# Kernel optimization log

Measured on AMD Instinct MI355X. Metric: run time of the kernel, lower is better.

## Reference

```python
import jax, jax.numpy as jnp
import numpy as np

COS_EPS = 1e-6   # torch CosineSimilarity eps
NORM_EPS = 1e-10 # assignment-normalizer eps


def setup_inputs() -> dict:
    key = jax.random.key(0)
    ks = jax.random.split(key, 12)
    s = 0.1
    H, K, Din, Dout = 8, 128, 64, 64
    return {
        "node_set": jax.random.normal(ks[0], (32, Din, 1024, 12), jnp.float32),
        "adj": jax.random.uniform(ks[1], (32, 1024, 1024), jnp.float32),
        "W0": jax.random.normal(ks[2], (Din, Din), jnp.float32) * s,
        "w_i2c": jax.random.normal(ks[3], (H, 1), jnp.float32) * s,
        "b_i2c": jax.random.normal(ks[4], (H,), jnp.float32) * s,
        "W_lin": jax.random.normal(ks[5], (H * K, H), jnp.float32) * s,
        "b_lin": jax.random.normal(ks[6], (H * K,), jnp.float32) * s,
        "conv_w": jax.random.normal(ks[7], (H,), jnp.float32) * s,
        "conv_b": jax.random.normal(ks[8], (), jnp.float32) * s,
        "W_feat": jax.random.normal(ks[9], (Dout, Din), jnp.float32) * s,
        "b_feat": jax.random.normal(ks[10], (Dout,), jnp.float32) * s,
    }


def reference(node_set, adj, W0, w_i2c, b_i2c, W_lin, b_lin, conv_w, conv_b, W_feat, b_feat):
    # [B, C, N, T] -> [B, N, C, T] -> mean over T -> [B, N, D]
    x = jnp.mean(jnp.transpose(node_set, (0, 2, 1, 3)), axis=3)
    B = x.shape[0]
    H = w_i2c.shape[0]
    K = W_lin.shape[0] // H

    # get_att: attention-pooled global centroid seed [B, 1, D]
    temp = jnp.mean(x, axis=1, keepdims=True)                 # [B,1,D]
    h_avg = jnp.tanh(jnp.einsum('bod,de->boe', temp, W0))    # [B,1,D]
    att = jnp.einsum('bnd,bod->bno', x, h_avg)               # [B,N,1]
    cent = jnp.einsum('bno,bnd->bod', att, x)                # [B,1,D]

    # generate batch centroids: [B,D,1] -> [B,D,H] -> [B,D,H*K] -> [B,H,K,D]
    bc = jnp.transpose(cent, (0, 2, 1))                       # [B,D,1]
    bc = jax.nn.relu(bc @ w_i2c.T + b_i2c)                    # [B,D,H]
    bc = jax.nn.relu(bc @ W_lin.T + b_lin)                    # [B,D,H*K]
    bc = jnp.transpose(bc, (0, 2, 1)).reshape(B, H, K, -1)    # [B,H,K,D]

    # cosine-similarity assignment (no 5D repeat: dot / max(|x||c|, eps))
    dots = jnp.einsum('bnd,bhkd->bhkn', x, bc)                # [B,H,K,N]
    xn = jnp.linalg.norm(x, axis=-1)                          # [B,N]
    cn = jnp.linalg.norm(bc, axis=-1)                         # [B,H,K]
    C_heads = dots / jnp.maximum(cn[..., None] * xn[:, None, None, :], COS_EPS)
    # normalize over centroids dim (dim 2)
    C_heads = C_heads / (jnp.sum(C_heads, axis=2, keepdims=True) + NORM_EPS)

    # 1x1 conv over heads -> single assignment matrix [B,K,N]
    C = jnp.einsum('h,bhkn->bkn', conv_w, C_heads) + conv_b

    # pooled node features + output projection
    new_node_set = jnp.einsum('bkn,bnd->bkd', C, x)           # [B,K,D]
    return new_node_set @ W_feat.T + b_feat                   # [B,K,Dout]
```

## Files before the change

### kernel.cpp

```cpp
#include <hip/hip_runtime.h>
#include <math.h>

#define B_  32
#define N_  1024
#define D_  64
#define H_  8
#define K_  128
#define HK_ 1024

__global__ __launch_bounds__(512) void k1_mean(const float* __restrict__ ns,
        float* __restrict__ x, float* __restrict__ invxn,
        float* __restrict__ part1) {
    __shared__ float tile[64][65];
    int b    = blockIdx.x >> 4;
    int n0   = (blockIdx.x & 15) << 6;
    int lane = threadIdx.x & 63;
    int w    = threadIdx.x >> 6;
    #pragma unroll
    for (int j = 0; j < 8; ++j) {
        int d = w * 8 + j;
        const float4* p = (const float4*)(ns +
            ((size_t)((b * 64 + d) * 1024 + n0 + lane)) * 12);
        float4 a = p[0], c = p[1], e = p[2];
        float s = ((a.x + a.y) + (a.z + a.w)) + ((c.x + c.y) + (c.z + c.w))
                + ((e.x + e.y) + (e.z + e.w));
        tile[lane][d] = s * (1.0f / 12.0f);
    }
    __syncthreads();
    #pragma unroll
    for (int j = 0; j < 8; ++j) {
        int r = w * 8 + j;
        float v = tile[r][lane];
        x[((size_t)(b * 1024 + n0 + r)) * 64 + lane] = v;
        float ss = v * v;
        #pragma unroll
        for (int o = 32; o; o >>= 1) ss += __shfl_xor(ss, o);
        if (lane == 0) invxn[b * 1024 + n0 + r] = 1.0f / sqrtf(fmaxf(ss, 1e-30f));
    }
    if (threadIdx.x < 64) {
        float s = 0.0f;
        #pragma unroll 16
        for (int r = 0; r < 64; ++r) s += tile[r][threadIdx.x];
        part1[(size_t)blockIdx.x * 64 + threadIdx.x] = s;
    }
}

__global__ __launch_bounds__(256) void k3_cent(const float* __restrict__ x,
        const float* __restrict__ part1, const float* __restrict__ W0,
        float* __restrict__ part2) {
    __shared__ float t[64];
    __shared__ float ha[64];
    __shared__ float cp[4][64];
    int b    = blockIdx.x >> 2;
    int n0   = (blockIdx.x & 3) << 8;
    int lane = threadIdx.x & 63;
    int w    = threadIdx.x >> 6;
    if (threadIdx.x < 64) {
        float s = 0.0f;
        #pragma unroll
        for (int j = 0; j < 16; ++j) s += part1[(size_t)(b * 16 + j) * 64 + threadIdx.x];
        t[threadIdx.x] = s * (1.0f / 1024.0f);
    }
    __syncthreads();
    if (threadIdx.x < 64) {
        float a = 0.0f;
        #pragma unroll 8
        for (int d = 0; d < 64; ++d) a += t[d] * W0[d * 64 + threadIdx.x];
        ha[threadIdx.x] = tanhf(a);
    }
    __syncthreads();
    float hv = ha[lane];
    float cw = 0.0f;
    for (int nn = w; nn < 256; nn += 4) {
        float xv = x[((size_t)(b * 1024 + n0 + nn)) * 64 + lane];
        float d  = xv * hv;
        #pragma unroll
        for (int o = 32; o; o >>= 1) d += __shfl_xor(d, o);
        cw += d * xv;
    }
    cp[w][lane] = cw;
    __syncthreads();
    if (w == 0)
        part2[(size_t)blockIdx.x * 64 + lane] =
            ((cp[0][lane] + cp[1][lane]) + (cp[2][lane] + cp[3][lane]));
}

__global__ __launch_bounds__(256) void k4_bc(const float* __restrict__ part2,
        const float* __restrict__ w_i2c, const float* __restrict__ b_i2c,
        const float* __restrict__ W_lin, const float* __restrict__ b_lin,
        float* __restrict__ bc, float* __restrict__ invcn) {
    int lane = threadIdx.x & 63;
    int w    = threadIdx.x >> 6;
    int gg   = blockIdx.x * 4 + w;
    int b    = gg >> 8;
    int kk0  = (gg & 255) * 4;
    float c = 0.0f;
    #pragma unroll
    for (int s = 0; s < 4; ++s) c += part2[(size_t)(b * 4 + s) * 64 + lane];
    float b1[8];
    #pragma unroll
    for (int h = 0; h < 8; ++h) b1[h] = fmaxf(c * w_i2c[h] + b_i2c[h], 0.0f);
    #pragma unroll
    for (int u = 0; u < 4; ++u) {
        int kk = kk0 + u;
        float pre = b_lin[kk];
        #pragma unroll
        for (int h = 0; h < 8; ++h) pre += b1[h] * W_lin[kk * 8 + h];
        float v = fmaxf(pre, 0.0f);
        bc[((size_t)(b * 1024 + kk)) * 64 + lane] = v;
        float ss = v * v;
        #pragma unroll
        for (int o = 32; o; o >>= 1) ss += __shfl_xor(ss, o);
        if (lane == 0) invcn[b * 1024 + kk] = (ss > 0.0f) ? (1.0f / sqrtf(ss)) : 0.0f;
    }
}

__global__ __launch_bounds__(256, 2) void k5_assign(const float* __restrict__ x,
        const float* __restrict__ bc, const float* __restrict__ invxn,
        const float* __restrict__ invcn, const float* __restrict__ conv_w,
        const float* __restrict__ conv_b, float* __restrict__ C) {
    __shared__ float xt[64][68];
    __shared__ float bct[128][68];
    __shared__ float invx_s[64];
    __shared__ float invc_s[128];
    __shared__ float sred[16][68];
    int b   = blockIdx.x >> 4;
    int n0  = (blockIdx.x & 15) << 6;
    int tid = threadIdx.x;
    {
        int r = tid >> 2, dh = (tid & 3) << 4;
        const float4* src = (const float4*)(x + ((size_t)(b * 1024 + n0 + r)) * 64 + dh);
        float4* dst = (float4*)(&xt[r][dh]);
        dst[0] = src[0]; dst[1] = src[1]; dst[2] = src[2]; dst[3] = src[3];
    }
    if (tid < 64) invx_s[tid] = invxn[b * 1024 + n0 + tid];
    {
        int r = tid >> 1, dh = (tid & 1) << 5;
        const float4* src = (const float4*)(bc + ((size_t)(b * 1024 + r)) * 64 + dh);
        float4* dst = (float4*)(&bct[r][dh]);
        #pragma unroll
        for (int u = 0; u < 8; ++u) dst[u] = src[u];
    }
    if (tid < 128) invc_s[tid] = invcn[b * 1024 + tid];
    float Cacc[8][4];
    #pragma unroll
    for (int i = 0; i < 8; ++i)
        #pragma unroll
        for (int j = 0; j < 4; ++j) Cacc[i][j] = 0.0f;
    int q = tid >> 4, p = tid & 15;
    float cb = conv_b[0];
    int rr = tid >> 1, dhh = (tid & 1) << 5;
    for (int h = 0; h < 8; ++h) {
        __syncthreads();
        int hn = (h + 1) & 7;
        float4 pf[8];
        float  pfc = 0.0f;
        {
            const float4* src = (const float4*)(bc + ((size_t)(b * 1024 + hn * 128 + rr)) * 64 + dhh);
            #pragma unroll
            for (int u = 0; u < 8; ++u) pf[u] = src[u];
        }
        if (tid < 128) pfc = invcn[b * 1024 + hn * 128 + tid];
        float acc[8][4];
        #pragma unroll
        for (int i = 0; i < 8; ++i)
            #pragma unroll
            for (int j = 0; j < 4; ++j) acc[i][j] = 0.0f;
        for (int dc = 0; dc < 64; dc += 4) {
            float4 bv[8], xv[4];
            #pragma unroll
            for (int i = 0; i < 8; ++i) bv[i] = *(const float4*)(&bct[q + 16 * i][dc]);
            #pragma unroll
            for (int j = 0; j < 4; ++j) xv[j] = *(const float4*)(&xt[p + 16 * j][dc]);
            #pragma unroll
            for (int i = 0; i < 8; ++i)
                #pragma unroll
                for (int j = 0; j < 4; ++j)
                    acc[i][j] += bv[i].x * xv[j].x + bv[i].y * xv[j].y
                               + bv[i].z * xv[j].z + bv[i].w * xv[j].w;
        }
        float part[4];
        #pragma unroll
        for (int j = 0; j < 4; ++j) part[j] = 0.0f;
        #pragma unroll
        for (int i = 0; i < 8; ++i) {
            float ic = invc_s[q + 16 * i];
            #pragma unroll
            for (int j = 0; j < 4; ++j) {
                float v = acc[i][j] * ic * invx_s[p + 16 * j];
                acc[i][j] = v;
                part[j] += v;
            }
        }
        #pragma unroll
        for (int j = 0; j < 4; ++j) sred[q][p + 16 * j] = part[j];
        __syncthreads();
        {
            float4* dst = (float4*)(&bct[rr][dhh]);
            #pragma unroll
            for (int u = 0; u < 8; ++u) dst[u] = pf[u];
        }
        if (tid < 128) invc_s[tid] = pfc;
        float cwv = conv_w[h];
        #pragma unroll
        for (int j = 0; j < 4; ++j) {
            float s = 0.0f;
            #pragma unroll
            for (int qq = 0; qq < 16; ++qq) s += sred[qq][p + 16 * j];
            float si = 1.0f / (s + 1e-10f);
            #pragma unroll
            for (int i = 0; i < 8; ++i) Cacc[i][j] += cwv * acc[i][j] * si;
        }
    }
    #pragma unroll
    for (int i = 0; i < 8; ++i) {
        int k = q + 16 * i;
        #pragma unroll
        for (int j = 0; j < 4; ++j)
            C[((size_t)(b * 128 + k)) * 1024 + n0 + p + 16 * j] = Cacc[i][j] + cb;
    }
}

__global__ __launch_bounds__(256, 2) void k6_out(const float* __restrict__ C,
        const float* __restrict__ x, const float* __restrict__ Wf,
        const float* __restrict__ bfeat, float* __restrict__ out) {
    __shared__ float xt[128][68];
    __shared__ float ct[16][132];
    __shared__ float nnst[16][68];
    __shared__ float wfs[64][68];
    int b   = blockIdx.x >> 3;
    int k0  = (blockIdx.x & 7) << 4;
    int tid = threadIdx.x;
    int kq  = tid >> 4, p = tid & 15;
    for (int t = tid; t < 4096; t += 256) wfs[t >> 6][t & 63] = Wf[t];
    float acc[4] = {0.0f, 0.0f, 0.0f, 0.0f};
    for (int c = 0; c < 8; ++c) {
        __syncthreads();
        {
            int r = tid >> 1, dh = (tid & 1) << 5;
            const float4* src = (const float4*)(x + ((size_t)(b * 1024 + c * 128 + r)) * 64 + dh);
            float4* dst = (float4*)(&xt[r][dh]);
            #pragma unroll
            for (int u = 0; u < 8; ++u) dst[u] = src[u];
        }
        for (int t = tid; t < 2048; t += 256)
            ct[t >> 7][t & 127] = C[((size_t)(b * 128 + k0 + (t >> 7))) * 1024 + c * 128 + (t & 127)];
        __syncthreads();
        #pragma unroll 8
        for (int n = 0; n < 128; ++n) {
            float  cv = ct[kq][n];
            float4 xv = *(const float4*)(&xt[n][p << 2]);
            acc[0] += cv * xv.x; acc[1] += cv * xv.y;
            acc[2] += cv * xv.z; acc[3] += cv * xv.w;
        }
    }
    __syncthreads();
    nnst[kq][(p << 2) + 0] = acc[0];
    nnst[kq][(p << 2) + 1] = acc[1];
    nnst[kq][(p << 2) + 2] = acc[2];
    nnst[kq][(p << 2) + 3] = acc[3];
    __syncthreads();
    float o0 = bfeat[(p << 2) + 0], o1 = bfeat[(p << 2) + 1];
    float o2 = bfeat[(p << 2) + 2], o3 = bfeat[(p << 2) + 3];
    #pragma unroll
    for (int dc = 0; dc < 64; dc += 4) {
        float4 nv = *(const float4*)(&nnst[kq][dc]);
        float4 w0 = *(const float4*)(&wfs[(p << 2) + 0][dc]);
        float4 w1 = *(const float4*)(&wfs[(p << 2) + 1][dc]);
        float4 w2 = *(const float4*)(&wfs[(p << 2) + 2][dc]);
        float4 w3 = *(const float4*)(&wfs[(p << 2) + 3][dc]);
        o0 += nv.x * w0.x + nv.y * w0.y + nv.z * w0.z + nv.w * w0.w;
        o1 += nv.x * w1.x + nv.y * w1.y + nv.z * w1.z + nv.w * w1.w;
        o2 += nv.x * w2.x + nv.y * w2.y + nv.z * w2.z + nv.w * w2.w;
        o3 += nv.x * w3.x + nv.y * w3.y + nv.z * w3.z + nv.w * w3.w;
    }
    float4 ov = make_float4(o0, o1, o2, o3);
    *(float4*)(out + ((size_t)(b * 128 + k0 + kq)) * 64 + (p << 2)) = ov;
}

extern "C" void kernel_launch(void* const* d_in, const int* in_sizes, int n_in,
                              void* d_out, int out_size, void* d_ws, size_t ws_size,
                              hipStream_t stream) {
    const float* node_set = (const float*)d_in[0];
    const float* W0     = (const float*)d_in[2];
    const float* w_i2c  = (const float*)d_in[3];
    const float* b_i2c  = (const float*)d_in[4];
    const float* W_lin  = (const float*)d_in[5];
    const float* b_lin  = (const float*)d_in[6];
    const float* conv_w = (const float*)d_in[7];
    const float* conv_b = (const float*)d_in[8];
    const float* W_feat = (const float*)d_in[9];
    const float* b_feat = (const float*)d_in[10];
    float* out = (float*)d_out;
    float* ws  = (float*)d_ws;

    float* x     = ws;
    float* invxn = ws + 2097152;
    float* part1 = ws + 2129920;
    float* part2 = ws + 2162688;
    float* bc    = ws + 2170880;
    float* invcn = ws + 4268032;
    float* Cmat  = ws + 4300800;

    k1_mean  <<<B_ * 16, 512, 0, stream>>>(node_set, x, invxn, part1);
    k3_cent  <<<B_ * 4,  256, 0, stream>>>(x, part1, W0, part2);
    k4_bc    <<<2048,    256, 0, stream>>>(part2, w_i2c, b_i2c, W_lin, b_lin, bc, invcn);
    k5_assign<<<B_ * 16, 256, 0, stream>>>(x, bc, invxn, invcn, conv_w, conv_b, Cmat);
    k6_out   <<<B_ * 8,  256, 0, stream>>>(Cmat, x, W_feat, b_feat, out);
}
```

Before: 419.1 us.

## Enlarge assign tile to 128 nodes with async LDS double-buffered centroid loads

```diff
diff --git a/kernel.cpp b/kernel.cpp
--- a/kernel.cpp
+++ b/kernel.cpp
@@ -7,6 +7,9 @@
 #define H_  8
 #define K_  128
 #define HK_ 1024
+
+#define GLB(p) ((const __attribute__((address_space(1))) void*)(p))
+#define LDSP(p) ((__attribute__((address_space(3))) void*)(p))
 
 __global__ __launch_bounds__(512) void k1_mean(const float* __restrict__ ns,
         float* __restrict__ x, float* __restrict__ invxn,
@@ -51,8 +54,8 @@
     __shared__ float t[64];
     __shared__ float ha[64];
     __shared__ float cp[4][64];
-    int b    = blockIdx.x >> 2;
-    int n0   = (blockIdx.x & 3) << 8;
+    int b    = blockIdx.x >> 3;
+    int n0   = (blockIdx.x & 7) << 7;
     int lane = threadIdx.x & 63;
     int w    = threadIdx.x >> 6;
     if (threadIdx.x < 64) {
@@ -71,7 +74,7 @@
     __syncthreads();
     float hv = ha[lane];
     float cw = 0.0f;
-    for (int nn = w; nn < 256; nn += 4) {
+    for (int nn = w; nn < 128; nn += 4) {
         float xv = x[((size_t)(b * 1024 + n0 + nn)) * 64 + lane];
         float d  = xv * hv;
         #pragma unroll
@@ -96,7 +99,7 @@
     int kk0  = (gg & 255) * 4;
     float c = 0.0f;
     #pragma unroll
-    for (int s = 0; s < 4; ++s) c += part2[(size_t)(b * 4 + s) * 64 + lane];
+    for (int s = 0; s < 8; ++s) c += part2[(size_t)(b * 8 + s) * 64 + lane];
     float b1[8];
     #pragma unroll
     for (int h = 0; h < 8; ++h) b1[h] = fmaxf(c * w_i2c[h] + b_i2c[h], 0.0f);
@@ -115,108 +118,141 @@
     }
 }
 
-__global__ __launch_bounds__(256, 2) void k5_assign(const float* __restrict__ x,
+__global__ __launch_bounds__(256, 1) void k5_assign(const float* __restrict__ x,
         const float* __restrict__ bc, const float* __restrict__ invxn,
         const float* __restrict__ invcn, const float* __restrict__ conv_w,
         const float* __restrict__ conv_b, float* __restrict__ C) {
-    __shared__ float xt[64][68];
-    __shared__ float bct[128][68];
-    __shared__ float invx_s[64];
-    __shared__ float invc_s[128];
-    __shared__ float sred[16][68];
-    int b   = blockIdx.x >> 4;
-    int n0  = (blockIdx.x & 15) << 6;
+    __shared__ float xt[128][68];
+    __shared__ float bct[2][128 * 64];
+    __shared__ float invx_s[128];
+    __shared__ float invc_s[2][128];
+    __shared__ float sredW[128][4];
+    int b   = blockIdx.x >> 3;
+    int n0  = (blockIdx.x & 7) << 7;
     int tid = threadIdx.x;
+    int l   = tid & 63, w = tid >> 6;
+    int q   = tid >> 4, p = tid & 15;
+    int rxor = q & 7;
+    int rl  = l >> 4, cl = l & 15;
     {
-        int r = tid >> 2, dh = (tid & 3) << 4;
+        int r = tid >> 1, dh = (tid & 1) << 5;
         const float4* src = (const float4*)(x + ((size_t)(b * 1024 + n0 + r)) * 64 + dh);
         float4* dst = (float4*)(&xt[r][dh]);
-        dst[0] = src[0]; dst[1] = src[1]; dst[2] = src[2]; dst[3] = src[3];
-    }
-    if (tid < 64) invx_s[tid] = invxn[b * 1024 + n0 + tid];
+        #pragma unroll
+        for (int u = 0; u < 8; ++u) dst[u] = src[u];
+    }
+    if (tid < 128) {
+        invx_s[tid]    = invxn[b * 1024 + n0 + tid];
+        invc_s[0][tid] = invcn[b * 1024 + tid];
+    }
     {
-        int r = tid >> 1, dh = (tid & 1) << 5;
-        const float4* src = (const float4*)(bc + ((size_t)(b * 1024 + r)) * 64 + dh);
-        float4* dst = (float4*)(&bct[r][dh]);
-        #pragma unroll
-        for (int u = 0; u < 8; ++u) dst[u] = src[u];
-    }
-    if (tid < 128) invc_s[tid] = invcn[b * 1024 + tid];
-    float Cacc[8][4];
+        const float* hb = bc + ((size_t)(b * 1024)) * 64;
+        #pragma unroll
+        for (int t = 0; t < 8; ++t) {
+            int chunk = w * 8 + t;
+            int r = chunk * 4 + rl;
+            const float* src = hb + (size_t)r * 64 + ((cl ^ (r & 7)) << 2);
+            __builtin_amdgcn_global_load_lds(GLB(src), LDSP(&bct[0][chunk * 256]), 16, 0, 0);
+        }
+    }
+    float Cacc[8][8];
     #pragma unroll
     for (int i = 0; i < 8; ++i)
         #pragma unroll
-        for (int j = 0; j < 4; ++j) Cacc[i][j] = 0.0f;
-    int q = tid >> 4, p = tid & 15;
+        for (int j = 0; j < 8; ++j) Cacc[i][j] = 0.0f;
     float cb = conv_b[0];
-    int rr = tid >> 1, dhh = (tid & 1) << 5;
+    __syncthreads();
+
     for (int h = 0; h < 8; ++h) {
-        __syncthreads();
-        int hn = (h + 1) & 7;
-        float4 pf[8];
-        float  pfc = 0.0f;
-        {
-            const float4* src = (const float4*)(bc + ((size_t)(b * 1024 + hn * 128 + rr)) * 64 + dhh);
-            #pragma unroll
-            for (int u = 0; u < 8; ++u) pf[u] = src[u];
-        }
-        if (tid < 128) pfc = invcn[b * 1024 + hn * 128 + tid];
-        float acc[8][4];
+        int cur = h & 1, nxt = cur ^ 1;
+        float pfc = 0.0f;
+        if (h < 7) {
+            const float* hb = bc + ((size_t)(b * 1024 + (h + 1) * 128)) * 64;
+            #pragma unroll
+            for (int t = 0; t < 8; ++t) {
+                int chunk = w * 8 + t;
+                int r = chunk * 4 + rl;
+                const float* src = hb + (size_t)r * 64 + ((cl ^ (r & 7)) << 2);
+                __builtin_amdgcn_global_load_lds(GLB(src), LDSP(&bct[nxt][chunk * 256]), 16, 0, 0);
+            }
+            if (tid < 128) pfc = invcn[b * 1024 + (h + 1) * 128 + tid];
+        }
+        const float4* B4 = (const float4*)(&bct[cur][0]);
+        float acc[8][8];
         #pragma unroll
         for (int i = 0; i < 8; ++i)
             #pragma unroll
-            for (int j = 0; j < 4; ++j) acc[i][j] = 0.0f;
-        for (int dc = 0; dc < 64; dc += 4) {
-            float4 bv[8], xv[4];
-            #pragma unroll
-            for (int i = 0; i < 8; ++i) bv[i] = *(const float4*)(&bct[q + 16 * i][dc]);
-            #pragma unroll
-            for (int j = 0; j < 4; ++j) xv[j] = *(const float4*)(&xt[p + 16 * j][dc]);
+            for (int j = 0; j < 8; ++j) acc[i][j] = 0.0f;
+        float4 bvA[8], xvA[8], bvB[8], xvB[8];
+        #pragma unroll
+        for (int i = 0; i < 8; ++i) bvA[i] = B4[(q + 16 * i) * 16 + (0 ^ rxor)];
+        #pragma unroll
+        for (int j = 0; j < 8; ++j) xvA[j] = *(const float4*)(&xt[p + 16 * j][0]);
+        #pragma unroll 1
+        for (int c = 0; c < 16; c += 2) {
+            #pragma unroll
+            for (int i = 0; i < 8; ++i) bvB[i] = B4[(q + 16 * i) * 16 + ((c + 1) ^ rxor)];
+            #pragma unroll
+            for (int j = 0; j < 8; ++j) xvB[j] = *(const float4*)(&xt[p + 16 * j][(c + 1) << 2]);
             #pragma unroll
             for (int i = 0; i < 8; ++i)
                 #pragma unroll
-                for (int j = 0; j < 4; ++j)
-                    acc[i][j] += bv[i].x * xv[j].x + bv[i].y * xv[j].y
-                               + bv[i].z * xv[j].z + bv[i].w * xv[j].w;
-        }
-        float part[4];
-        #pragma unroll
-        for (int j = 0; j < 4; ++j) part[j] = 0.0f;
+                for (int j = 0; j < 8; ++j)
+                    acc[i][j] += bvA[i].x * xvA[j].x + bvA[i].y * xvA[j].y
+                               + bvA[i].z * xvA[j].z + bvA[i].w * xvA[j].w;
+            if (c + 2 < 16) {
+                #pragma unroll
+                for (int i = 0; i < 8; ++i) bvA[i] = B4[(q + 16 * i) * 16 + ((c + 2) ^ rxor)];
+                #pragma unroll
+                for (int j = 0; j < 8; ++j) xvA[j] = *(const float4*)(&xt[p + 16 * j][(c + 2) << 2]);
+            }
+            #pragma unroll
+            for (int i = 0; i < 8; ++i)
+                #pragma unroll
+                for (int j = 0; j < 8; ++j)
+                    acc[i][j] += bvB[i].x * xvB[j].x + bvB[i].y * xvB[j].y
+                               + bvB[i].z * xvB[j].z + bvB[i].w * xvB[j].w;
+        }
+        float part[8];
+        #pragma unroll
+        for (int j = 0; j < 8; ++j) part[j] = 0.0f;
         #pragma unroll
         for (int i = 0; i < 8; ++i) {
-            float ic = invc_s[q + 16 * i];
-            #pragma unroll
-            for (int j = 0; j < 4; ++j) {
+            float ic = invc_s[cur][q + 16 * i];
+            #pragma unroll
+            for (int j = 0; j < 8; ++j) {
                 float v = acc[i][j] * ic * invx_s[p + 16 * j];
                 acc[i][j] = v;
                 part[j] += v;
             }
         }
         #pragma unroll
-        for (int j = 0; j < 4; ++j) sred[q][p + 16 * j] = part[j];
+        for (int j = 0; j < 8; ++j) {
+            part[j] += __shfl_xor(part[j], 16);
+            part[j] += __shfl_xor(part[j], 32);
+        }
+        if (l < 16) {
+            #pragma unroll
+            for (int j = 0; j < 8; ++j) sredW[p + 16 * j][w] = part[j];
+        }
         __syncthreads();
-        {
-            float4* dst = (float4*)(&bct[rr][dhh]);
-            #pragma unroll
-            for (int u = 0; u < 8; ++u) dst[u] = pf[u];
-        }
-        if (tid < 128) invc_s[tid] = pfc;
+        if (h < 7 && tid < 128) invc_s[nxt][tid] = pfc;
         float cwv = conv_w[h];
         #pragma unroll
-        for (int j = 0; j < 4; ++j) {
-            float s = 0.0f;
-            #pragma unroll
-            for (int qq = 0; qq < 16; ++qq) s += sred[qq][p + 16 * j];
+        for (int j = 0; j < 8; ++j) {
+            float4 sv = *(const float4*)(&sredW[p + 16 * j][0]);
+            float s  = (sv.x + sv.y) + (sv.z + sv.w);
             float si = 1.0f / (s + 1e-10f);
             #pragma unroll
             for (int i = 0; i < 8; ++i) Cacc[i][j] += cwv * acc[i][j] * si;
         }
+        __syncthreads();
     }
     #pragma unroll
     for (int i = 0; i < 8; ++i) {
         int k = q + 16 * i;
         #pragma unroll
-        for (int j = 0; j < 4; ++j)
+        for (int j = 0; j < 8; ++j)
             C[((size_t)(b * 128 + k)) * 1024 + n0 + p + 16 * j] = Cacc[i][j] + cb;
     }
 }
@@ -297,14 +333,14 @@
     float* x     = ws;
     float* invxn = ws + 2097152;
     float* part1 = ws + 2129920;
-    float* part2 = ws + 2162688;
-    float* bc    = ws + 2170880;
-    float* invcn = ws + 4268032;
-    float* Cmat  = ws + 4300800;
+    float* bc    = ws + 2162688;
+    float* invcn = ws + 4259840;
+    float* Cmat  = ws + 4292608;
+    float* part2 = Cmat;
 
     k1_mean  <<<B_ * 16, 512, 0, stream>>>(node_set, x, invxn, part1);
-    k3_cent  <<<B_ * 4,  256, 0, stream>>>(x, part1, W0, part2);
+    k3_cent  <<<B_ * 8,  256, 0, stream>>>(x, part1, W0, part2);
     k4_bc    <<<2048,    256, 0, stream>>>(part2, w_i2c, b_i2c, W_lin, b_lin, bc, invcn);
-    k5_assign<<<B_ * 16, 256, 0, stream>>>(x, bc, invxn, invcn, conv_w, conv_b, Cmat);
+    k5_assign<<<B_ * 8,  256, 0, stream>>>(x, bc, invxn, invcn, conv_w, conv_b, Cmat);
     k6_out   <<<B_ * 8,  256, 0, stream>>>(Cmat, x, W_feat, b_feat, out);
 }
```

Result: faster. 396.0 us (-5.5%).
